# Optimization experiments

Measured on AMD Instinct MI355X. Metric: run time of the kernel, lower is better.

## Reference

```python
import jax, jax.numpy as jnp
import numpy as np

HEAD_SIZE = 64  # n_embds // n_heads = 1024 // 16

def setup_inputs() -> dict:
    key = jax.random.key(0)
    k0, k1, k2, k3 = jax.random.split(key, 4)
    B, S, D, H = 4, 4096, 1024, HEAD_SIZE
    scale = 1.0 / np.sqrt(D)
    return {
        "decoder_input": jax.random.normal(k0, (B, S, D), dtype=jnp.float32),
        "Wq": jax.random.normal(k1, (D, H), dtype=jnp.float32) * scale,
        "Wk": jax.random.normal(k2, (D, H), dtype=jnp.float32) * scale,
        "Wv": jax.random.normal(k3, (D, H), dtype=jnp.float32) * scale,
    }

def reference(decoder_input, Wq, Wk, Wv):
    # q,k,v: [B,S,H]; Linear(bias=False) == x @ W
    q = decoder_input @ Wq
    k = decoder_input @ Wk
    v = decoder_input @ Wv
    head_size = k.shape[2]
    # scores: [B,S,S] -- full materialization, as in the original
    scores = jnp.einsum('bqh,bkh->bqk', q, k) / jnp.sqrt(jnp.float32(head_size))
    S = scores.shape[1]
    causal = jnp.tril(jnp.ones((S, S), dtype=bool))  # lower-triangular mask
    masked = jnp.where(causal, scores, -jnp.inf)
    attn = jax.nn.softmax(masked, axis=2)
    # dropout_rate = 0.0 -> identity
    return jnp.einsum('bqk,bkh->bqh', attn, v)
```

## Files before the change

kernel.cpp:

```cpp
#include <hip/hip_runtime.h>
#include <hip/hip_bf16.h>
#include <math.h>

typedef __bf16 bf16_t;
typedef __bf16 bf16x8 __attribute__((ext_vector_type(8)));
typedef float f32x4 __attribute__((ext_vector_type(4)));

constexpr int SS = 4096;
constexpr int DD = 1024;
constexpr int HH = 64;

#if __has_builtin(__builtin_amdgcn_exp2f)
#define EXP2F __builtin_amdgcn_exp2f
#else
#define EXP2F exp2f
#endif

static __device__ __forceinline__ f32x4 mfma16(bf16x8 a, bf16x8 b, f32x4 c) {
  return __builtin_amdgcn_mfma_f32_16x16x32_bf16(a, b, c, 0, 0, 0);
}

__global__ __launch_bounds__(256) void prep_w(const float* __restrict__ wq,
                                              const float* __restrict__ wk,
                                              const float* __restrict__ wv,
                                              bf16_t* __restrict__ wt) {
  __shared__ float ls[64 * 68];
  int tid = threadIdx.x;
  int sel = blockIdx.x >> 4, kb = blockIdx.x & 15, k0 = kb * 64;
  const float* src = (sel == 0) ? wq : ((sel == 1) ? wk : wv);
  int bn = sel * 64;
#pragma unroll
  for (int i = 0; i < 4; ++i) {
    int e = tid + i * 256;
    int r = e >> 4, c4 = (e & 15) * 4;
    *(float4*)&ls[r * 68 + c4] = *(const float4*)(src + (size_t)(k0 + r) * 64 + c4);
  }
  __syncthreads();
#pragma unroll
  for (int j = 0; j < 2; ++j) {
    int e = tid + j * 256;
    int n = e >> 3, kg = e & 7;
    bf16x8 v;
#pragma unroll
    for (int t = 0; t < 8; ++t) v[t] = (bf16_t)ls[(kg * 8 + t) * 68 + n];
    *(bf16x8*)(wt + (size_t)(bn + n) * 1024 + k0 + kg * 8) = v;
  }
}

__global__ __launch_bounds__(256) void gemm_qkv(const float* __restrict__ x,
                                                const bf16_t* __restrict__ wt,
                                                bf16_t* __restrict__ qo,
                                                bf16_t* __restrict__ ko,
                                                bf16_t* __restrict__ vto) {
  __shared__ bf16_t xs[2][32 * 64];
  __shared__ bf16_t wsh[2][96 * 64];
  int tid = threadIdx.x;
  int wave = tid >> 6, lane = tid & 63, quad = lane >> 4, ml = lane & 15;
  int mh = wave >> 1, nh = wave & 1;
  int mblk = blockIdx.x >> 1, nhalf = blockIdx.x & 1;
  int m0 = mblk * 32;
  int nbase = nhalf * 96;

  f32x4 acc[3];
#pragma unroll
  for (int i = 0; i < 3; ++i) acc[i] = (f32x4){0.f, 0.f, 0.f, 0.f};

  int srow = tid >> 3, scc = tid & 7;
  float4 xr[2];
  bf16x8 wr[3];

  auto load_g = [&](int k0) {
    const float* p = x + (size_t)(m0 + srow) * DD + k0 + scc * 8;
    xr[0] = *(const float4*)p;
    xr[1] = *(const float4*)(p + 4);
#pragma unroll
    for (int i = 0; i < 3; ++i) {
      int c = tid + i * 256;
      int r = c >> 3, cc = c & 7;
      wr[i] = *(const bf16x8*)(wt + (size_t)(nbase + r) * DD + k0 + cc * 8);
    }
  };
  auto store_lds = [&](int bf) {
    bf16x8 v;
    v[0] = (bf16_t)xr[0].x; v[1] = (bf16_t)xr[0].y;
    v[2] = (bf16_t)xr[0].z; v[3] = (bf16_t)xr[0].w;
    v[4] = (bf16_t)xr[1].x; v[5] = (bf16_t)xr[1].y;
    v[6] = (bf16_t)xr[1].z; v[7] = (bf16_t)xr[1].w;
    *(bf16x8*)&xs[bf][srow * 64 + ((scc ^ (srow & 7)) * 8)] = v;
#pragma unroll
    for (int i = 0; i < 3; ++i) {
      int c = tid + i * 256;
      int r = c >> 3, cc = c & 7;
      *(bf16x8*)&wsh[bf][r * 64 + ((cc ^ (r & 7)) * 8)] = wr[i];
    }
  };

  load_g(0);
  store_lds(0);
  load_g(64);
  __syncthreads();
  for (int it = 0; it < 16; ++it) {
    int bf = it & 1;
#pragma unroll
    for (int s = 0; s < 2; ++s) {
      int rchunk = ((s * 4 + quad) ^ (ml & 7)) * 8;
      bf16x8 a = *(const bf16x8*)&xs[bf][(mh * 16 + ml) * 64 + rchunk];
#pragma unroll
      for (int i = 0; i < 3; ++i) {
        bf16x8 bfr = *(const bf16x8*)&wsh[bf][(nh * 48 + i * 16 + ml) * 64 + rchunk];
        acc[i] = mfma16(a, bfr, acc[i]);
      }
    }
    if (it < 15) {
      store_lds(1 - bf);
      if (it < 14) load_g((it + 2) * 64);
      __syncthreads();
    }
  }

  int b = m0 >> 12;
  int sr = m0 & 4095;
  const float QSCALE = 0.18033688011112042f;
  bf16_t* vls = (bf16_t*)xs;
  __syncthreads();
#pragma unroll
  for (int i = 0; i < 3; ++i) {
    int col = nbase + nh * 48 + i * 16 + ml;
#pragma unroll
    for (int r = 0; r < 4; ++r) {
      int lrow = mh * 16 + quad * 4 + r;
      size_t grow = (size_t)b * SS + sr + lrow;
      if (col < 64) qo[grow * HH + col] = (bf16_t)(acc[i][r] * QSCALE);
      else if (col < 128) ko[grow * HH + (col - 64)] = (bf16_t)(acc[i][r]);
      else vls[(col - 128) * 40 + lrow] = (bf16_t)(acc[i][r]);
    }
  }
  if (nhalf == 1) {
    __syncthreads();
    int h = tid >> 2, sg = tid & 3;
    *(bf16x8*)(vto + ((size_t)b * HH + h) * SS + sr + sg * 8) =
        *(const bf16x8*)&vls[h * 40 + sg * 8];
  }
}

__global__ __launch_bounds__(256) void attn_partial(const bf16_t* __restrict__ qg,
                                                    const bf16_t* __restrict__ kg,
                                                    const bf16_t* __restrict__ vg,
                                                    float* __restrict__ partO,
                                                    float* __restrict__ lb,
                                                    float* __restrict__ out) {
  __shared__ bf16_t Kl[64 * 64];
  __shared__ bf16_t Vl[64 * 64];
  __shared__ bf16_t Pl[4][16 * 64];
  int tid = threadIdx.x;
  int wave = tid >> 6, lane = tid & 63, quad = lane >> 4, ml = lane & 15;

  int bid = blockIdx.x;
  int b, jt, c0, len, slot = 0;
  bool direct;
  if (bid < 768) {
    jt = 63 - (bid >> 4);
    int rem = bid & 15;
    b = rem >> 2;
    int ch = rem & 3;
    int L = (jt + 4) >> 2;
    c0 = ch * L;
    int c1 = c0 + L; if (c1 > jt + 1) c1 = jt + 1;
    len = c1 - c0;
    slot = (b * 48 + (jt - 16)) * 4 + ch;
    direct = false;
  } else {
    int idx = bid - 768;
    jt = 15 - (idx >> 2);
    b = idx & 3;
    c0 = 0;
    len = jt + 1;
    direct = true;
  }
  int q0 = jt * 64;

  const bf16_t* qb = qg + (size_t)b * SS * HH;
  const bf16_t* kb = kg + (size_t)b * SS * HH;
  const bf16_t* vb = vg + (size_t)b * HH * SS;

  int qrow = q0 + wave * 16 + ml;
  bf16x8 aq0 = *(const bf16x8*)(qb + (size_t)qrow * HH + quad * 8);
  bf16x8 aq1 = *(const bf16x8*)(qb + (size_t)qrow * HH + 32 + quad * 8);

  bf16x8 kreg[2], vreg[2];
  int srl = tid >> 3, scc = tid & 7;
  auto load_kv = [&](int kt) {
#pragma unroll
    for (int i = 0; i < 2; ++i) {
      int r = srl + i * 32;
      kreg[i] = *(const bf16x8*)(kb + (size_t)(kt * 64 + r) * HH + scc * 8);
      vreg[i] = *(const bf16x8*)(vb + (size_t)r * SS + kt * 64 + scc * 8);
    }
  };
  auto store_kv = [&]() {
#pragma unroll
    for (int i = 0; i < 2; ++i) {
      int r = srl + i * 32;
      int off = r * 64 + ((scc ^ (r & 7)) * 8);
      *(bf16x8*)&Kl[off] = kreg[i];
      *(bf16x8*)&Vl[off] = vreg[i];
    }
  };

  f32x4 oa[4];
#pragma unroll
  for (int i = 0; i < 4; ++i) oa[i] = (f32x4){0.f, 0.f, 0.f, 0.f};
  float lr[4] = {0.f, 0.f, 0.f, 0.f};

  load_kv(c0);
  store_kv();

  for (int i = 0; i < len; ++i) {
    int kt = c0 + i;
    __syncthreads();
    if (i + 1 < len) load_kv(kt + 1);

    f32x4 sa[4];
#pragma unroll
    for (int nt = 0; nt < 4; ++nt) sa[nt] = (f32x4){0.f, 0.f, 0.f, 0.f};
#pragma unroll
    for (int s = 0; s < 2; ++s) {
      bf16x8 a = s ? aq1 : aq0;
      int rchunk = ((s * 4 + quad) ^ (ml & 7)) * 8;
#pragma unroll
      for (int nt = 0; nt < 4; ++nt) {
        bf16x8 bfr = *(const bf16x8*)&Kl[(nt * 16 + ml) * 64 + rchunk];
        sa[nt] = mfma16(a, bfr, sa[nt]);
      }
    }

    if (kt == jt) {
#pragma unroll
      for (int nt = 0; nt < 4; ++nt) {
        int key = kt * 64 + nt * 16 + ml;
#pragma unroll
        for (int r = 0; r < 4; ++r) {
          int qr = q0 + wave * 16 + quad * 4 + r;
          if (key > qr) sa[nt][r] = -3.38953139e38f;
        }
      }
    }

#pragma unroll
    for (int r = 0; r < 4; ++r) {
      float p0 = EXP2F(sa[0][r]);
      float p1 = EXP2F(sa[1][r]);
      float p2 = EXP2F(sa[2][r]);
      float p3 = EXP2F(sa[3][r]);
      sa[0][r] = p0; sa[1][r] = p1; sa[2][r] = p2; sa[3][r] = p3;
      lr[r] += (p0 + p1) + (p2 + p3);
    }

#pragma unroll
    for (int nt = 0; nt < 4; ++nt) {
#pragma unroll
      for (int r = 0; r < 4; ++r) {
        int row = quad * 4 + r;
        int cc = nt * 2 + (ml >> 3);
        Pl[wave][row * 64 + ((cc ^ (row & 7)) * 8) + (ml & 7)] = (bf16_t)sa[nt][r];
      }
    }
#pragma unroll
    for (int s = 0; s < 2; ++s) {
      int rchunk = ((s * 4 + quad) ^ (ml & 7)) * 8;
      bf16x8 pa = *(const bf16x8*)&Pl[wave][ml * 64 + rchunk];
#pragma unroll
      for (int ht = 0; ht < 4; ++ht) {
        bf16x8 bv = *(const bf16x8*)&Vl[(ht * 16 + ml) * 64 + rchunk];
        oa[ht] = mfma16(pa, bv, oa[ht]);
      }
    }

    __syncthreads();
    if (i + 1 < len) store_kv();
  }

#pragma unroll
  for (int r = 0; r < 4; ++r) {
    float t = lr[r];
    t += __shfl_xor(t, 1);
    t += __shfl_xor(t, 2);
    t += __shfl_xor(t, 4);
    t += __shfl_xor(t, 8);
    lr[r] = t;
  }

  if (direct) {
#pragma unroll
    for (int r = 0; r < 4; ++r) {
      float inv = 1.0f / lr[r];
      int row = q0 + wave * 16 + quad * 4 + r;
#pragma unroll
      for (int ht = 0; ht < 4; ++ht)
        out[((size_t)b * SS + row) * HH + ht * 16 + ml] = oa[ht][r] * inv;
    }
  } else {
    float* po = partO + (size_t)slot * 4096;
#pragma unroll
    for (int r = 0; r < 4; ++r) {
      int row = wave * 16 + quad * 4 + r;
#pragma unroll
      for (int ht = 0; ht < 4; ++ht)
        po[row * 64 + ht * 16 + ml] = oa[ht][r];
      if (ml == 0) lb[slot * 64 + row] = lr[r];
    }
  }
}

__global__ __launch_bounds__(256) void combine(const float* __restrict__ partO,
                                               const float* __restrict__ lb,
                                               float* __restrict__ out) {
  int bid = blockIdx.x;
  int b = bid / 96;
  int rest = bid - b * 96;
  int jt = 16 + (rest >> 1), half = rest & 1;
  int base = (b * 48 + (jt - 16)) * 4;
  int tid = threadIdx.x;
  int lr_ = tid >> 3, cb = tid & 7;
  int row = half * 32 + lr_;

  float l = 0.f;
  float4 o0 = {0.f, 0.f, 0.f, 0.f}, o1 = {0.f, 0.f, 0.f, 0.f};
#pragma unroll
  for (int c = 0; c < 4; ++c) {
    l += lb[(base + c) * 64 + row];
    const float* p = partO + (size_t)(base + c) * 4096 + row * 64 + cb * 8;
    float4 a = *(const float4*)p;
    float4 bq = *(const float4*)(p + 4);
    o0.x += a.x; o0.y += a.y; o0.z += a.z; o0.w += a.w;
    o1.x += bq.x; o1.y += bq.y; o1.z += bq.z; o1.w += bq.w;
  }
  float inv = 1.0f / l;
  float* op = out + (((size_t)b * SS) + jt * 64 + row) * HH + cb * 8;
  o0.x *= inv; o0.y *= inv; o0.z *= inv; o0.w *= inv;
  o1.x *= inv; o1.y *= inv; o1.z *= inv; o1.w *= inv;
  *(float4*)op = o0;
  *(float4*)(op + 4) = o1;
}

extern "C" void kernel_launch(void* const* d_in, const int* in_sizes, int n_in,
                              void* d_out, int out_size, void* d_ws, size_t ws_size,
                              hipStream_t stream) {
  const float* x  = (const float*)d_in[0];
  const float* wq = (const float*)d_in[1];
  const float* wk = (const float*)d_in[2];
  const float* wv = (const float*)d_in[3];
  float* out = (float*)d_out;

  char* wsb = (char*)d_ws;
  bf16_t* wt  = (bf16_t*)wsb;
  bf16_t* q   = (bf16_t*)(wsb + 524288);
  bf16_t* k   = (bf16_t*)(wsb + 2621440);
  bf16_t* vt  = (bf16_t*)(wsb + 4718592);
  float*  po  = (float*)(wsb + 6815744);
  float*  lb  = (float*)(wsb + 19398656);

  prep_w<<<48, 256, 0, stream>>>(wq, wk, wv, wt);
  gemm_qkv<<<1024, 256, 0, stream>>>(x, wt, q, k, vt);
  attn_partial<<<832, 256, 0, stream>>>(q, k, vt, po, lb, out);
  combine<<<384, 256, 0, stream>>>(po, lb, out);
}
```

Baseline: 155.8 us.

## Split attention KV into fixed 8-tile chunks with double-buffered LDS

```diff
diff --git a/kernel.cpp b/kernel.cpp
--- a/kernel.cpp
+++ b/kernel.cpp
@@ -149,34 +149,21 @@
                                                     float* __restrict__ partO,
                                                     float* __restrict__ lb,
                                                     float* __restrict__ out) {
-  __shared__ bf16_t Kl[64 * 64];
-  __shared__ bf16_t Vl[64 * 64];
+  __shared__ bf16_t Kl[2][64 * 64];
+  __shared__ bf16_t Vl[2][64 * 64];
   __shared__ bf16_t Pl[4][16 * 64];
   int tid = threadIdx.x;
   int wave = tid >> 6, lane = tid & 63, quad = lane >> 4, ml = lane & 15;
 
   int bid = blockIdx.x;
-  int b, jt, c0, len, slot = 0;
-  bool direct;
-  if (bid < 768) {
-    jt = 63 - (bid >> 4);
-    int rem = bid & 15;
-    b = rem >> 2;
-    int ch = rem & 3;
-    int L = (jt + 4) >> 2;
-    c0 = ch * L;
-    int c1 = c0 + L; if (c1 > jt + 1) c1 = jt + 1;
-    len = c1 - c0;
-    slot = (b * 48 + (jt - 16)) * 4 + ch;
-    direct = false;
-  } else {
-    int idx = bid - 768;
-    jt = 15 - (idx >> 2);
-    b = idx & 3;
-    c0 = 0;
-    len = jt + 1;
-    direct = true;
-  }
+  int jt = 63 - (bid >> 5);
+  int b = (bid >> 3) & 3;
+  int ch = bid & 7;
+  int nch = (jt >> 3) + 1;
+  if (ch >= nch) return;
+  int c0 = ch * 8;
+  int len = min(8, jt + 1 - c0);
+  bool direct = (nch == 1);
   int q0 = jt * 64;
 
   const bf16_t* qb = qg + (size_t)b * SS * HH;
@@ -197,13 +184,13 @@
       vreg[i] = *(const bf16x8*)(vb + (size_t)r * SS + kt * 64 + scc * 8);
     }
   };
-  auto store_kv = [&]() {
+  auto store_kv = [&](int bf) {
 #pragma unroll
     for (int i = 0; i < 2; ++i) {
       int r = srl + i * 32;
       int off = r * 64 + ((scc ^ (r & 7)) * 8);
-      *(bf16x8*)&Kl[off] = kreg[i];
-      *(bf16x8*)&Vl[off] = vreg[i];
+      *(bf16x8*)&Kl[bf][off] = kreg[i];
+      *(bf16x8*)&Vl[bf][off] = vreg[i];
     }
   };
 
@@ -213,10 +200,11 @@
   float lr[4] = {0.f, 0.f, 0.f, 0.f};
 
   load_kv(c0);
-  store_kv();
+  store_kv(0);
 
   for (int i = 0; i < len; ++i) {
     int kt = c0 + i;
+    int bf = i & 1;
     __syncthreads();
     if (i + 1 < len) load_kv(kt + 1);
 
@@ -229,7 +217,7 @@
       int rchunk = ((s * 4 + quad) ^ (ml & 7)) * 8;
 #pragma unroll
       for (int nt = 0; nt < 4; ++nt) {
-        bf16x8 bfr = *(const bf16x8*)&Kl[(nt * 16 + ml) * 64 + rchunk];
+        bf16x8 bfr = *(const bf16x8*)&Kl[bf][(nt * 16 + ml) * 64 + rchunk];
         sa[nt] = mfma16(a, bfr, sa[nt]);
       }
     }
@@ -271,13 +259,12 @@
       bf16x8 pa = *(const bf16x8*)&Pl[wave][ml * 64 + rchunk];
 #pragma unroll
       for (int ht = 0; ht < 4; ++ht) {
-        bf16x8 bv = *(const bf16x8*)&Vl[(ht * 16 + ml) * 64 + rchunk];
+        bf16x8 bv = *(const bf16x8*)&Vl[bf][(ht * 16 + ml) * 64 + rchunk];
         oa[ht] = mfma16(pa, bv, oa[ht]);
       }
     }
 
-    __syncthreads();
-    if (i + 1 < len) store_kv();
+    if (i + 1 < len) store_kv(1 - bf);
   }
 
 #pragma unroll
@@ -300,6 +287,7 @@
         out[((size_t)b * SS + row) * HH + ht * 16 + ml] = oa[ht][r] * inv;
     }
   } else {
+    int slot = (b << 9) + (jt << 3) + ch;
     float* po = partO + (size_t)slot * 4096;
 #pragma unroll
     for (int r = 0; r < 4; ++r) {
@@ -316,31 +304,27 @@
                                                const float* __restrict__ lb,
                                                float* __restrict__ out) {
   int bid = blockIdx.x;
-  int b = bid / 96;
-  int rest = bid - b * 96;
-  int jt = 16 + (rest >> 1), half = rest & 1;
-  int base = (b * 48 + (jt - 16)) * 4;
+  int b = bid / 56;
+  int jt = 8 + (bid - b * 56);
+  int nch = (jt >> 3) + 1;
+  int base = (b << 9) + (jt << 3);
   int tid = threadIdx.x;
-  int lr_ = tid >> 3, cb = tid & 7;
-  int row = half * 32 + lr_;
+  int row = tid >> 2, cb = tid & 3;
 
   float l = 0.f;
-  float4 o0 = {0.f, 0.f, 0.f, 0.f}, o1 = {0.f, 0.f, 0.f, 0.f};
-#pragma unroll
-  for (int c = 0; c < 4; ++c) {
+  f32x4 o[4];
+#pragma unroll
+  for (int j = 0; j < 4; ++j) o[j] = (f32x4){0.f, 0.f, 0.f, 0.f};
+  for (int c = 0; c < nch; ++c) {
     l += lb[(base + c) * 64 + row];
-    const float* p = partO + (size_t)(base + c) * 4096 + row * 64 + cb * 8;
-    float4 a = *(const float4*)p;
-    float4 bq = *(const float4*)(p + 4);
-    o0.x += a.x; o0.y += a.y; o0.z += a.z; o0.w += a.w;
-    o1.x += bq.x; o1.y += bq.y; o1.z += bq.z; o1.w += bq.w;
+    const f32x4* p = (const f32x4*)(partO + (size_t)(base + c) * 4096 + row * 64 + cb * 16);
+#pragma unroll
+    for (int j = 0; j < 4; ++j) o[j] += p[j];
   }
   float inv = 1.0f / l;
-  float* op = out + (((size_t)b * SS) + jt * 64 + row) * HH + cb * 8;
-  o0.x *= inv; o0.y *= inv; o0.z *= inv; o0.w *= inv;
-  o1.x *= inv; o1.y *= inv; o1.z *= inv; o1.w *= inv;
-  *(float4*)op = o0;
-  *(float4*)(op + 4) = o1;
+  f32x4* op = (f32x4*)(out + (((size_t)b * SS) + jt * 64 + row) * HH + cb * 16);
+#pragma unroll
+  for (int j = 0; j < 4; ++j) op[j] = o[j] * inv;
 }
 
 extern "C" void kernel_launch(void* const* d_in, const int* in_sizes, int n_in,
@@ -358,10 +342,10 @@
   bf16_t* k   = (bf16_t*)(wsb + 2621440);
   bf16_t* vt  = (bf16_t*)(wsb + 4718592);
   float*  po  = (float*)(wsb + 6815744);
-  float*  lb  = (float*)(wsb + 19398656);
+  float*  lb  = (float*)(wsb + 40370176);
 
   prep_w<<<48, 256, 0, stream>>>(wq, wk, wv, wt);
   gemm_qkv<<<1024, 256, 0, stream>>>(x, wt, q, k, vt);
-  attn_partial<<<832, 256, 0, stream>>>(q, k, vt, po, lb, out);
-  combine<<<384, 256, 0, stream>>>(po, lb, out);
-}
+  attn_partial<<<2048, 256, 0, stream>>>(q, k, vt, po, lb, out);
+  combine<<<224, 256, 0, stream>>>(po, lb, out);
+}
```

After: 160.7 us. 1.03x slower.

## Enlarge QKV GEMM M-tile to 64 rows and double-buffer K/V in attention

Applied to the files above, without the earlier changes.

```diff
diff --git a/kernel.cpp b/kernel.cpp
--- a/kernel.cpp
+++ b/kernel.cpp
@@ -52,27 +52,28 @@
                                                 bf16_t* __restrict__ qo,
                                                 bf16_t* __restrict__ ko,
                                                 bf16_t* __restrict__ vto) {
-  __shared__ bf16_t xs[2][32 * 64];
+  __shared__ bf16_t xs[2][64 * 64];
   __shared__ bf16_t wsh[2][96 * 64];
   int tid = threadIdx.x;
   int wave = tid >> 6, lane = tid & 63, quad = lane >> 4, ml = lane & 15;
-  int mh = wave >> 1, nh = wave & 1;
   int mblk = blockIdx.x >> 1, nhalf = blockIdx.x & 1;
-  int m0 = mblk * 32;
+  int m0 = mblk * 64;
   int nbase = nhalf * 96;
 
-  f32x4 acc[3];
-#pragma unroll
-  for (int i = 0; i < 3; ++i) acc[i] = (f32x4){0.f, 0.f, 0.f, 0.f};
-
-  int srow = tid >> 3, scc = tid & 7;
-  float4 xr[2];
+  f32x4 acc[6];
+#pragma unroll
+  for (int i = 0; i < 6; ++i) acc[i] = (f32x4){0.f, 0.f, 0.f, 0.f};
+
+  int xrow = tid >> 2, xseg = tid & 3;
+  float4 xr[4];
   bf16x8 wr[3];
 
   auto load_g = [&](int k0) {
-    const float* p = x + (size_t)(m0 + srow) * DD + k0 + scc * 8;
+    const float* p = x + (size_t)(m0 + xrow) * DD + k0 + xseg * 16;
     xr[0] = *(const float4*)p;
     xr[1] = *(const float4*)(p + 4);
+    xr[2] = *(const float4*)(p + 8);
+    xr[3] = *(const float4*)(p + 12);
 #pragma unroll
     for (int i = 0; i < 3; ++i) {
       int c = tid + i * 256;
@@ -81,12 +82,19 @@
     }
   };
   auto store_lds = [&](int bf) {
-    bf16x8 v;
-    v[0] = (bf16_t)xr[0].x; v[1] = (bf16_t)xr[0].y;
-    v[2] = (bf16_t)xr[0].z; v[3] = (bf16_t)xr[0].w;
-    v[4] = (bf16_t)xr[1].x; v[5] = (bf16_t)xr[1].y;
-    v[6] = (bf16_t)xr[1].z; v[7] = (bf16_t)xr[1].w;
-    *(bf16x8*)&xs[bf][srow * 64 + ((scc ^ (srow & 7)) * 8)] = v;
+    bf16x8 v0, v1;
+    v0[0] = (bf16_t)xr[0].x; v0[1] = (bf16_t)xr[0].y;
+    v0[2] = (bf16_t)xr[0].z; v0[3] = (bf16_t)xr[0].w;
+    v0[4] = (bf16_t)xr[1].x; v0[5] = (bf16_t)xr[1].y;
+    v0[6] = (bf16_t)xr[1].z; v0[7] = (bf16_t)xr[1].w;
+    v1[0] = (bf16_t)xr[2].x; v1[1] = (bf16_t)xr[2].y;
+    v1[2] = (bf16_t)xr[2].z; v1[3] = (bf16_t)xr[2].w;
+    v1[4] = (bf16_t)xr[3].x; v1[5] = (bf16_t)xr[3].y;
+    v1[6] = (bf16_t)xr[3].z; v1[7] = (bf16_t)xr[3].w;
+    int cc0 = (2 * xseg) ^ (xrow & 7);
+    int cc1 = (2 * xseg + 1) ^ (xrow & 7);
+    *(bf16x8*)&xs[bf][xrow * 64 + cc0 * 8] = v0;
+    *(bf16x8*)&xs[bf][xrow * 64 + cc1 * 8] = v1;
 #pragma unroll
     for (int i = 0; i < 3; ++i) {
       int c = tid + i * 256;
@@ -104,10 +112,10 @@
 #pragma unroll
     for (int s = 0; s < 2; ++s) {
       int rchunk = ((s * 4 + quad) ^ (ml & 7)) * 8;
-      bf16x8 a = *(const bf16x8*)&xs[bf][(mh * 16 + ml) * 64 + rchunk];
-#pragma unroll
-      for (int i = 0; i < 3; ++i) {
-        bf16x8 bfr = *(const bf16x8*)&wsh[bf][(nh * 48 + i * 16 + ml) * 64 + rchunk];
+      bf16x8 a = *(const bf16x8*)&xs[bf][(wave * 16 + ml) * 64 + rchunk];
+#pragma unroll
+      for (int i = 0; i < 6; ++i) {
+        bf16x8 bfr = *(const bf16x8*)&wsh[bf][(i * 16 + ml) * 64 + rchunk];
         acc[i] = mfma16(a, bfr, acc[i]);
       }
     }
@@ -121,25 +129,26 @@
   int b = m0 >> 12;
   int sr = m0 & 4095;
   const float QSCALE = 0.18033688011112042f;
-  bf16_t* vls = (bf16_t*)xs;
-  __syncthreads();
-#pragma unroll
-  for (int i = 0; i < 3; ++i) {
-    int col = nbase + nh * 48 + i * 16 + ml;
+  bf16_t* vls = (bf16_t*)wsh;
+#pragma unroll
+  for (int i = 0; i < 6; ++i) {
+    int col = nbase + i * 16 + ml;
 #pragma unroll
     for (int r = 0; r < 4; ++r) {
-      int lrow = mh * 16 + quad * 4 + r;
+      int lrow = wave * 16 + quad * 4 + r;
       size_t grow = (size_t)b * SS + sr + lrow;
       if (col < 64) qo[grow * HH + col] = (bf16_t)(acc[i][r] * QSCALE);
       else if (col < 128) ko[grow * HH + (col - 64)] = (bf16_t)(acc[i][r]);
-      else vls[(col - 128) * 40 + lrow] = (bf16_t)(acc[i][r]);
-    }
-  }
+      else vls[(col - 128) * 72 + lrow] = (bf16_t)(acc[i][r]);
+    }
+  }
+  __syncthreads();
   if (nhalf == 1) {
-    __syncthreads();
     int h = tid >> 2, sg = tid & 3;
-    *(bf16x8*)(vto + ((size_t)b * HH + h) * SS + sr + sg * 8) =
-        *(const bf16x8*)&vls[h * 40 + sg * 8];
+    *(bf16x8*)(vto + ((size_t)b * HH + h) * SS + sr + sg * 16) =
+        *(const bf16x8*)&vls[h * 72 + sg * 16];
+    *(bf16x8*)(vto + ((size_t)b * HH + h) * SS + sr + sg * 16 + 8) =
+        *(const bf16x8*)&vls[h * 72 + sg * 16 + 8];
   }
 }
 
@@ -149,8 +158,8 @@
                                                     float* __restrict__ partO,
                                                     float* __restrict__ lb,
                                                     float* __restrict__ out) {
-  __shared__ bf16_t Kl[64 * 64];
-  __shared__ bf16_t Vl[64 * 64];
+  __shared__ bf16_t Kl[2][64 * 64];
+  __shared__ bf16_t Vl[2][64 * 64];
   __shared__ bf16_t Pl[4][16 * 64];
   int tid = threadIdx.x;
   int wave = tid >> 6, lane = tid & 63, quad = lane >> 4, ml = lane & 15;
@@ -197,13 +206,13 @@
       vreg[i] = *(const bf16x8*)(vb + (size_t)r * SS + kt * 64 + scc * 8);
     }
   };
-  auto store_kv = [&]() {
+  auto store_kv = [&](int bf) {
 #pragma unroll
     for (int i = 0; i < 2; ++i) {
       int r = srl + i * 32;
       int off = r * 64 + ((scc ^ (r & 7)) * 8);
-      *(bf16x8*)&Kl[off] = kreg[i];
-      *(bf16x8*)&Vl[off] = vreg[i];
+      *(bf16x8*)&Kl[bf][off] = kreg[i];
+      *(bf16x8*)&Vl[bf][off] = vreg[i];
     }
   };
 
@@ -213,10 +222,11 @@
   float lr[4] = {0.f, 0.f, 0.f, 0.f};
 
   load_kv(c0);
-  store_kv();
+  store_kv(0);
 
   for (int i = 0; i < len; ++i) {
     int kt = c0 + i;
+    int bf = i & 1;
     __syncthreads();
     if (i + 1 < len) load_kv(kt + 1);
 
@@ -229,7 +239,7 @@
       int rchunk = ((s * 4 + quad) ^ (ml & 7)) * 8;
 #pragma unroll
       for (int nt = 0; nt < 4; ++nt) {
-        bf16x8 bfr = *(const bf16x8*)&Kl[(nt * 16 + ml) * 64 + rchunk];
+        bf16x8 bfr = *(const bf16x8*)&Kl[bf][(nt * 16 + ml) * 64 + rchunk];
         sa[nt] = mfma16(a, bfr, sa[nt]);
       }
     }
@@ -271,13 +281,12 @@
       bf16x8 pa = *(const bf16x8*)&Pl[wave][ml * 64 + rchunk];
 #pragma unroll
       for (int ht = 0; ht < 4; ++ht) {
-        bf16x8 bv = *(const bf16x8*)&Vl[(ht * 16 + ml) * 64 + rchunk];
+        bf16x8 bv = *(const bf16x8*)&Vl[bf][(ht * 16 + ml) * 64 + rchunk];
         oa[ht] = mfma16(pa, bv, oa[ht]);
       }
     }
 
-    __syncthreads();
-    if (i + 1 < len) store_kv();
+    if (i + 1 < len) store_kv(1 - bf);
   }
 
 #pragma unroll
@@ -361,7 +370,7 @@
   float*  lb  = (float*)(wsb + 19398656);
 
   prep_w<<<48, 256, 0, stream>>>(wq, wk, wv, wt);
-  gemm_qkv<<<1024, 256, 0, stream>>>(x, wt, q, k, vt);
+  gemm_qkv<<<512, 256, 0, stream>>>(x, wt, q, k, vt);
   attn_partial<<<832, 256, 0, stream>>>(q, k, vt, po, lb, out);
   combine<<<384, 256, 0, stream>>>(po, lb, out);
 }
```

New measurement: 151.4 us. 2.8% less time.

## Fuse all four stages into one cooperative persistent kernel with grid syncs

Applied to the files above, without the earlier changes.

```diff
diff --git a/kernel.cpp b/kernel.cpp
--- a/kernel.cpp
+++ b/kernel.cpp
@@ -1,6 +1,9 @@
 #include <hip/hip_runtime.h>
+#include <hip/hip_cooperative_groups.h>
 #include <hip/hip_bf16.h>
 #include <math.h>
+
+namespace cg = cooperative_groups;
 
 typedef __bf16 bf16_t;
 typedef __bf16 bf16x8 __attribute__((ext_vector_type(8)));
@@ -20,327 +23,341 @@
   return __builtin_amdgcn_mfma_f32_16x16x32_bf16(a, b, c, 0, 0, 0);
 }
 
-__global__ __launch_bounds__(256) void prep_w(const float* __restrict__ wq,
-                                              const float* __restrict__ wk,
-                                              const float* __restrict__ wv,
-                                              bf16_t* __restrict__ wt) {
-  __shared__ float ls[64 * 68];
-  int tid = threadIdx.x;
-  int sel = blockIdx.x >> 4, kb = blockIdx.x & 15, k0 = kb * 64;
-  const float* src = (sel == 0) ? wq : ((sel == 1) ? wk : wv);
-  int bn = sel * 64;
-#pragma unroll
-  for (int i = 0; i < 4; ++i) {
-    int e = tid + i * 256;
-    int r = e >> 4, c4 = (e & 15) * 4;
-    *(float4*)&ls[r * 68 + c4] = *(const float4*)(src + (size_t)(k0 + r) * 64 + c4);
-  }
-  __syncthreads();
-#pragma unroll
-  for (int j = 0; j < 2; ++j) {
-    int e = tid + j * 256;
-    int n = e >> 3, kg = e & 7;
-    bf16x8 v;
-#pragma unroll
-    for (int t = 0; t < 8; ++t) v[t] = (bf16_t)ls[(kg * 8 + t) * 68 + n];
-    *(bf16x8*)(wt + (size_t)(bn + n) * 1024 + k0 + kg * 8) = v;
-  }
-}
-
-__global__ __launch_bounds__(256) void gemm_qkv(const float* __restrict__ x,
-                                                const bf16_t* __restrict__ wt,
+__global__ __launch_bounds__(256, 4) void fused(const float* __restrict__ x,
+                                                const float* __restrict__ wq,
+                                                const float* __restrict__ wk,
+                                                const float* __restrict__ wv,
+                                                bf16_t* __restrict__ wt,
                                                 bf16_t* __restrict__ qo,
                                                 bf16_t* __restrict__ ko,
-                                                bf16_t* __restrict__ vto) {
-  __shared__ bf16_t xs[2][32 * 64];
-  __shared__ bf16_t wsh[2][96 * 64];
-  int tid = threadIdx.x;
-  int wave = tid >> 6, lane = tid & 63, quad = lane >> 4, ml = lane & 15;
-  int mh = wave >> 1, nh = wave & 1;
-  int mblk = blockIdx.x >> 1, nhalf = blockIdx.x & 1;
-  int m0 = mblk * 32;
-  int nbase = nhalf * 96;
-
-  f32x4 acc[3];
-#pragma unroll
-  for (int i = 0; i < 3; ++i) acc[i] = (f32x4){0.f, 0.f, 0.f, 0.f};
-
-  int srow = tid >> 3, scc = tid & 7;
-  float4 xr[2];
-  bf16x8 wr[3];
-
-  auto load_g = [&](int k0) {
-    const float* p = x + (size_t)(m0 + srow) * DD + k0 + scc * 8;
-    xr[0] = *(const float4*)p;
-    xr[1] = *(const float4*)(p + 4);
-#pragma unroll
-    for (int i = 0; i < 3; ++i) {
-      int c = tid + i * 256;
-      int r = c >> 3, cc = c & 7;
-      wr[i] = *(const bf16x8*)(wt + (size_t)(nbase + r) * DD + k0 + cc * 8);
-    }
-  };
-  auto store_lds = [&](int bf) {
-    bf16x8 v;
-    v[0] = (bf16_t)xr[0].x; v[1] = (bf16_t)xr[0].y;
-    v[2] = (bf16_t)xr[0].z; v[3] = (bf16_t)xr[0].w;
-    v[4] = (bf16_t)xr[1].x; v[5] = (bf16_t)xr[1].y;
-    v[6] = (bf16_t)xr[1].z; v[7] = (bf16_t)xr[1].w;
-    *(bf16x8*)&xs[bf][srow * 64 + ((scc ^ (srow & 7)) * 8)] = v;
-#pragma unroll
-    for (int i = 0; i < 3; ++i) {
-      int c = tid + i * 256;
-      int r = c >> 3, cc = c & 7;
-      *(bf16x8*)&wsh[bf][r * 64 + ((cc ^ (r & 7)) * 8)] = wr[i];
-    }
-  };
-
-  load_g(0);
-  store_lds(0);
-  load_g(64);
-  __syncthreads();
-  for (int it = 0; it < 16; ++it) {
-    int bf = it & 1;
-#pragma unroll
-    for (int s = 0; s < 2; ++s) {
-      int rchunk = ((s * 4 + quad) ^ (ml & 7)) * 8;
-      bf16x8 a = *(const bf16x8*)&xs[bf][(mh * 16 + ml) * 64 + rchunk];
-#pragma unroll
-      for (int i = 0; i < 3; ++i) {
-        bf16x8 bfr = *(const bf16x8*)&wsh[bf][(nh * 48 + i * 16 + ml) * 64 + rchunk];
-        acc[i] = mfma16(a, bfr, acc[i]);
-      }
-    }
-    if (it < 15) {
-      store_lds(1 - bf);
-      if (it < 14) load_g((it + 2) * 64);
+                                                bf16_t* __restrict__ vto,
+                                                float* __restrict__ partO,
+                                                float* __restrict__ lb,
+                                                float* __restrict__ out) {
+  __shared__ __align__(16) char smem[40960];
+  cg::grid_group grid = cg::this_grid();
+  const int nwg = gridDim.x;
+  const int wg = blockIdx.x;
+  const int tid = threadIdx.x;
+  const int wave = tid >> 6, lane = tid & 63, quad = lane >> 4, ml = lane & 15;
+
+  {
+    float* ls = (float*)smem;
+    for (int job = wg; job < 48; job += nwg) {
+      int sel = job >> 4, kb = job & 15, k0 = kb * 64;
+      const float* src = (sel == 0) ? wq : ((sel == 1) ? wk : wv);
+      int bn = sel * 64;
+#pragma unroll
+      for (int i = 0; i < 4; ++i) {
+        int e = tid + i * 256;
+        int r = e >> 4, c4 = (e & 15) * 4;
+        *(float4*)&ls[r * 68 + c4] = *(const float4*)(src + (size_t)(k0 + r) * 64 + c4);
+      }
+      __syncthreads();
+#pragma unroll
+      for (int j = 0; j < 2; ++j) {
+        int e = tid + j * 256;
+        int n = e >> 3, kg = e & 7;
+        bf16x8 v;
+#pragma unroll
+        for (int t = 0; t < 8; ++t) v[t] = (bf16_t)ls[(kg * 8 + t) * 68 + n];
+        *(bf16x8*)(wt + (size_t)(bn + n) * 1024 + k0 + kg * 8) = v;
+      }
       __syncthreads();
     }
   }
-
-  int b = m0 >> 12;
-  int sr = m0 & 4095;
-  const float QSCALE = 0.18033688011112042f;
-  bf16_t* vls = (bf16_t*)xs;
-  __syncthreads();
-#pragma unroll
-  for (int i = 0; i < 3; ++i) {
-    int col = nbase + nh * 48 + i * 16 + ml;
-#pragma unroll
-    for (int r = 0; r < 4; ++r) {
-      int lrow = mh * 16 + quad * 4 + r;
-      size_t grow = (size_t)b * SS + sr + lrow;
-      if (col < 64) qo[grow * HH + col] = (bf16_t)(acc[i][r] * QSCALE);
-      else if (col < 128) ko[grow * HH + (col - 64)] = (bf16_t)(acc[i][r]);
-      else vls[(col - 128) * 40 + lrow] = (bf16_t)(acc[i][r]);
+  grid.sync();
+
+  {
+    bf16_t* xs = (bf16_t*)smem;
+    bf16_t* wsh = (bf16_t*)(smem + 8192);
+    int mh = wave >> 1, nh = wave & 1;
+    int srow = tid >> 3, scc = tid & 7;
+
+    for (int job = wg; job < 1024; job += nwg) {
+      int mblk = job >> 1, nhalf = job & 1;
+      int m0 = mblk * 32;
+      int nbase = nhalf * 96;
+
+      f32x4 acc[3];
+#pragma unroll
+      for (int i = 0; i < 3; ++i) acc[i] = (f32x4){0.f, 0.f, 0.f, 0.f};
+
+      float4 xr[2];
+      bf16x8 wr[3];
+
+      auto load_g = [&](int k0) {
+        const float* p = x + (size_t)(m0 + srow) * DD + k0 + scc * 8;
+        xr[0] = *(const float4*)p;
+        xr[1] = *(const float4*)(p + 4);
+#pragma unroll
+        for (int i = 0; i < 3; ++i) {
+          int c = tid + i * 256;
+          int r = c >> 3, cc = c & 7;
+          wr[i] = *(const bf16x8*)(wt + (size_t)(nbase + r) * DD + k0 + cc * 8);
+        }
+      };
+      auto store_lds = [&](int bf) {
+        bf16x8 v;
+        v[0] = (bf16_t)xr[0].x; v[1] = (bf16_t)xr[0].y;
+        v[2] = (bf16_t)xr[0].z; v[3] = (bf16_t)xr[0].w;
+        v[4] = (bf16_t)xr[1].x; v[5] = (bf16_t)xr[1].y;
+        v[6] = (bf16_t)xr[1].z; v[7] = (bf16_t)xr[1].w;
+        *(bf16x8*)&xs[bf * 2048 + srow * 64 + ((scc ^ (srow & 7)) * 8)] = v;
+#pragma unroll
+        for (int i = 0; i < 3; ++i) {
+          int c = tid + i * 256;
+          int r = c >> 3, cc = c & 7;
+          *(bf16x8*)&wsh[bf * 6144 + r * 64 + ((cc ^ (r & 7)) * 8)] = wr[i];
+        }
+      };
+
+      load_g(0);
+      __syncthreads();
+      store_lds(0);
+      load_g(64);
+      __syncthreads();
+      for (int it = 0; it < 16; ++it) {
+        int bf = it & 1;
+#pragma unroll
+        for (int s = 0; s < 2; ++s) {
+          int rchunk = ((s * 4 + quad) ^ (ml & 7)) * 8;
+          bf16x8 a = *(const bf16x8*)&xs[bf * 2048 + (mh * 16 + ml) * 64 + rchunk];
+#pragma unroll
+          for (int i = 0; i < 3; ++i) {
+            bf16x8 bfr =
+                *(const bf16x8*)&wsh[bf * 6144 + (nh * 48 + i * 16 + ml) * 64 + rchunk];
+            acc[i] = mfma16(a, bfr, acc[i]);
+          }
+        }
+        if (it < 15) {
+          store_lds(1 - bf);
+          if (it < 14) load_g((it + 2) * 64);
+          __syncthreads();
+        }
+      }
+
+      int b = m0 >> 12;
+      int sr = m0 & 4095;
+      const float QSCALE = 0.18033688011112042f;
+      bf16_t* vls = xs;
+      __syncthreads();
+#pragma unroll
+      for (int i = 0; i < 3; ++i) {
+        int col = nbase + nh * 48 + i * 16 + ml;
+#pragma unroll
+        for (int r = 0; r < 4; ++r) {
+          int lrow = mh * 16 + quad * 4 + r;
+          size_t grow = (size_t)b * SS + sr + lrow;
+          if (col < 64) qo[grow * HH + col] = (bf16_t)(acc[i][r] * QSCALE);
+          else if (col < 128) ko[grow * HH + (col - 64)] = (bf16_t)(acc[i][r]);
+          else vls[(col - 128) * 40 + lrow] = (bf16_t)(acc[i][r]);
+        }
+      }
+      __syncthreads();
+      if (nhalf == 1) {
+        int h = tid >> 2, sg = tid & 3;
+        *(bf16x8*)(vto + ((size_t)b * HH + h) * SS + sr + sg * 8) =
+            *(const bf16x8*)&vls[h * 40 + sg * 8];
+      }
     }
   }
-  if (nhalf == 1) {
-    __syncthreads();
-    int h = tid >> 2, sg = tid & 3;
-    *(bf16x8*)(vto + ((size_t)b * HH + h) * SS + sr + sg * 8) =
-        *(const bf16x8*)&vls[h * 40 + sg * 8];
-  }
-}
-
-__global__ __launch_bounds__(256) void attn_partial(const bf16_t* __restrict__ qg,
-                                                    const bf16_t* __restrict__ kg,
-                                                    const bf16_t* __restrict__ vg,
-                                                    float* __restrict__ partO,
-                                                    float* __restrict__ lb,
-                                                    float* __restrict__ out) {
-  __shared__ bf16_t Kl[64 * 64];
-  __shared__ bf16_t Vl[64 * 64];
-  __shared__ bf16_t Pl[4][16 * 64];
-  int tid = threadIdx.x;
-  int wave = tid >> 6, lane = tid & 63, quad = lane >> 4, ml = lane & 15;
-
-  int bid = blockIdx.x;
-  int b, jt, c0, len, slot = 0;
-  bool direct;
-  if (bid < 768) {
-    jt = 63 - (bid >> 4);
-    int rem = bid & 15;
-    b = rem >> 2;
-    int ch = rem & 3;
-    int L = (jt + 4) >> 2;
-    c0 = ch * L;
-    int c1 = c0 + L; if (c1 > jt + 1) c1 = jt + 1;
-    len = c1 - c0;
-    slot = (b * 48 + (jt - 16)) * 4 + ch;
-    direct = false;
-  } else {
-    int idx = bid - 768;
-    jt = 15 - (idx >> 2);
-    b = idx & 3;
-    c0 = 0;
-    len = jt + 1;
-    direct = true;
-  }
-  int q0 = jt * 64;
-
-  const bf16_t* qb = qg + (size_t)b * SS * HH;
-  const bf16_t* kb = kg + (size_t)b * SS * HH;
-  const bf16_t* vb = vg + (size_t)b * HH * SS;
-
-  int qrow = q0 + wave * 16 + ml;
-  bf16x8 aq0 = *(const bf16x8*)(qb + (size_t)qrow * HH + quad * 8);
-  bf16x8 aq1 = *(const bf16x8*)(qb + (size_t)qrow * HH + 32 + quad * 8);
-
-  bf16x8 kreg[2], vreg[2];
-  int srl = tid >> 3, scc = tid & 7;
-  auto load_kv = [&](int kt) {
-#pragma unroll
-    for (int i = 0; i < 2; ++i) {
-      int r = srl + i * 32;
-      kreg[i] = *(const bf16x8*)(kb + (size_t)(kt * 64 + r) * HH + scc * 8);
-      vreg[i] = *(const bf16x8*)(vb + (size_t)r * SS + kt * 64 + scc * 8);
-    }
-  };
-  auto store_kv = [&]() {
-#pragma unroll
-    for (int i = 0; i < 2; ++i) {
-      int r = srl + i * 32;
-      int off = r * 64 + ((scc ^ (r & 7)) * 8);
-      *(bf16x8*)&Kl[off] = kreg[i];
-      *(bf16x8*)&Vl[off] = vreg[i];
-    }
-  };
-
-  f32x4 oa[4];
-#pragma unroll
-  for (int i = 0; i < 4; ++i) oa[i] = (f32x4){0.f, 0.f, 0.f, 0.f};
-  float lr[4] = {0.f, 0.f, 0.f, 0.f};
-
-  load_kv(c0);
-  store_kv();
-
-  for (int i = 0; i < len; ++i) {
-    int kt = c0 + i;
-    __syncthreads();
-    if (i + 1 < len) load_kv(kt + 1);
-
-    f32x4 sa[4];
-#pragma unroll
-    for (int nt = 0; nt < 4; ++nt) sa[nt] = (f32x4){0.f, 0.f, 0.f, 0.f};
-#pragma unroll
-    for (int s = 0; s < 2; ++s) {
-      bf16x8 a = s ? aq1 : aq0;
-      int rchunk = ((s * 4 + quad) ^ (ml & 7)) * 8;
-#pragma unroll
-      for (int nt = 0; nt < 4; ++nt) {
-        bf16x8 bfr = *(const bf16x8*)&Kl[(nt * 16 + ml) * 64 + rchunk];
-        sa[nt] = mfma16(a, bfr, sa[nt]);
-      }
-    }
-
-    if (kt == jt) {
-#pragma unroll
-      for (int nt = 0; nt < 4; ++nt) {
-        int key = kt * 64 + nt * 16 + ml;
+  grid.sync();
+
+  {
+    bf16_t* Kl = (bf16_t*)smem;
+    bf16_t* Vl = (bf16_t*)(smem + 16384);
+    bf16_t* Pl = (bf16_t*)(smem + 32768);
+    int srl = tid >> 3, scc = tid & 7;
+
+    for (int job = wg; job < 832; job += nwg) {
+      int b, jt, c0, len, slot = 0;
+      bool direct;
+      if (job < 768) {
+        jt = 63 - (job >> 4);
+        int rem = job & 15;
+        b = rem >> 2;
+        int ch = rem & 3;
+        int L = (jt + 4) >> 2;
+        c0 = ch * L;
+        int c1 = c0 + L; if (c1 > jt + 1) c1 = jt + 1;
+        len = c1 - c0;
+        slot = (b * 48 + (jt - 16)) * 4 + ch;
+        direct = false;
+      } else {
+        int idx = job - 768;
+        jt = 15 - (idx >> 2);
+        b = idx & 3;
+        c0 = 0;
+        len = jt + 1;
+        direct = true;
+      }
+      int q0 = jt * 64;
+
+      const bf16_t* qb = qo + (size_t)b * SS * HH;
+      const bf16_t* kb = ko + (size_t)b * SS * HH;
+      const bf16_t* vb = vto + (size_t)b * HH * SS;
+
+      int qrow = q0 + wave * 16 + ml;
+      bf16x8 aq0 = *(const bf16x8*)(qb + (size_t)qrow * HH + quad * 8);
+      bf16x8 aq1 = *(const bf16x8*)(qb + (size_t)qrow * HH + 32 + quad * 8);
+
+      bf16x8 kreg[2], vreg[2];
+      auto load_kv = [&](int kt) {
+#pragma unroll
+        for (int i = 0; i < 2; ++i) {
+          int r = srl + i * 32;
+          kreg[i] = *(const bf16x8*)(kb + (size_t)(kt * 64 + r) * HH + scc * 8);
+          vreg[i] = *(const bf16x8*)(vb + (size_t)r * SS + kt * 64 + scc * 8);
+        }
+      };
+      auto store_kv = [&](int bf) {
+#pragma unroll
+        for (int i = 0; i < 2; ++i) {
+          int r = srl + i * 32;
+          int off = r * 64 + ((scc ^ (r & 7)) * 8);
+          *(bf16x8*)&Kl[bf * 4096 + off] = kreg[i];
+          *(bf16x8*)&Vl[bf * 4096 + off] = vreg[i];
+        }
+      };
+
+      f32x4 oa[4];
+#pragma unroll
+      for (int i = 0; i < 4; ++i) oa[i] = (f32x4){0.f, 0.f, 0.f, 0.f};
+      float lr[4] = {0.f, 0.f, 0.f, 0.f};
+
+      load_kv(c0);
+      __syncthreads();
+      store_kv(0);
+
+      for (int i = 0; i < len; ++i) {
+        int kt = c0 + i;
+        int bf = i & 1;
+        __syncthreads();
+        if (i + 1 < len) load_kv(kt + 1);
+
+        f32x4 sa[4];
+#pragma unroll
+        for (int nt = 0; nt < 4; ++nt) sa[nt] = (f32x4){0.f, 0.f, 0.f, 0.f};
+#pragma unroll
+        for (int s = 0; s < 2; ++s) {
+          bf16x8 a = s ? aq1 : aq0;
+          int rchunk = ((s * 4 + quad) ^ (ml & 7)) * 8;
+#pragma unroll
+          for (int nt = 0; nt < 4; ++nt) {
+            bf16x8 bfr = *(const bf16x8*)&Kl[bf * 4096 + (nt * 16 + ml) * 64 + rchunk];
+            sa[nt] = mfma16(a, bfr, sa[nt]);
+          }
+        }
+
+        if (kt == jt) {
+#pragma unroll
+          for (int nt = 0; nt < 4; ++nt) {
+            int key = kt * 64 + nt * 16 + ml;
+#pragma unroll
+            for (int r = 0; r < 4; ++r) {
+              int qr = q0 + wave * 16 + quad * 4 + r;
+              if (key > qr) sa[nt][r] = -3.38953139e38f;
+            }
+          }
+        }
+
 #pragma unroll
         for (int r = 0; r < 4; ++r) {
-          int qr = q0 + wave * 16 + quad * 4 + r;
-          if (key > qr) sa[nt][r] = -3.38953139e38f;
-        }
-      }
-    }
-
-#pragma unroll
-    for (int r = 0; r < 4; ++r) {
-      float p0 = EXP2F(sa[0][r]);
-      float p1 = EXP2F(sa[1][r]);
-      float p2 = EXP2F(sa[2][r]);
-      float p3 = EXP2F(sa[3][r]);
-      sa[0][r] = p0; sa[1][r] = p1; sa[2][r] = p2; sa[3][r] = p3;
-      lr[r] += (p0 + p1) + (p2 + p3);
-    }
-
-#pragma unroll
-    for (int nt = 0; nt < 4; ++nt) {
+          float p0 = EXP2F(sa[0][r]);
+          float p1 = EXP2F(sa[1][r]);
+          float p2 = EXP2F(sa[2][r]);
+          float p3 = EXP2F(sa[3][r]);
+          sa[0][r] = p0; sa[1][r] = p1; sa[2][r] = p2; sa[3][r] = p3;
+          lr[r] += (p0 + p1) + (p2 + p3);
+        }
+
+#pragma unroll
+        for (int nt = 0; nt < 4; ++nt) {
+#pragma unroll
+          for (int r = 0; r < 4; ++r) {
+            int row = quad * 4 + r;
+            int cc = nt * 2 + (ml >> 3);
+            Pl[wave * 1024 + row * 64 + ((cc ^ (row & 7)) * 8) + (ml & 7)] =
+                (bf16_t)sa[nt][r];
+          }
+        }
+#pragma unroll
+        for (int s = 0; s < 2; ++s) {
+          int rchunk = ((s * 4 + quad) ^ (ml & 7)) * 8;
+          bf16x8 pa = *(const bf16x8*)&Pl[wave * 1024 + ml * 64 + rchunk];
+#pragma unroll
+          for (int ht = 0; ht < 4; ++ht) {
+            bf16x8 bv = *(const bf16x8*)&Vl[bf * 4096 + (ht * 16 + ml) * 64 + rchunk];
+            oa[ht] = mfma16(pa, bv, oa[ht]);
+          }
+        }
+
+        if (i + 1 < len) store_kv(1 - bf);
+      }
+
 #pragma unroll
       for (int r = 0; r < 4; ++r) {
-        int row = quad * 4 + r;
-        int cc = nt * 2 + (ml >> 3);
-        Pl[wave][row * 64 + ((cc ^ (row & 7)) * 8) + (ml & 7)] = (bf16_t)sa[nt][r];
-      }
-    }
-#pragma unroll
-    for (int s = 0; s < 2; ++s) {
-      int rchunk = ((s * 4 + quad) ^ (ml & 7)) * 8;
-      bf16x8 pa = *(const bf16x8*)&Pl[wave][ml * 64 + rchunk];
-#pragma unroll
-      for (int ht = 0; ht < 4; ++ht) {
-        bf16x8 bv = *(const bf16x8*)&Vl[(ht * 16 + ml) * 64 + rchunk];
-        oa[ht] = mfma16(pa, bv, oa[ht]);
-      }
-    }
-
-    __syncthreads();
-    if (i + 1 < len) store_kv();
-  }
-
-#pragma unroll
-  for (int r = 0; r < 4; ++r) {
-    float t = lr[r];
-    t += __shfl_xor(t, 1);
-    t += __shfl_xor(t, 2);
-    t += __shfl_xor(t, 4);
-    t += __shfl_xor(t, 8);
-    lr[r] = t;
-  }
-
-  if (direct) {
-#pragma unroll
-    for (int r = 0; r < 4; ++r) {
-      float inv = 1.0f / lr[r];
-      int row = q0 + wave * 16 + quad * 4 + r;
-#pragma unroll
-      for (int ht = 0; ht < 4; ++ht)
-        out[((size_t)b * SS + row) * HH + ht * 16 + ml] = oa[ht][r] * inv;
-    }
-  } else {
-    float* po = partO + (size_t)slot * 4096;
-#pragma unroll
-    for (int r = 0; r < 4; ++r) {
-      int row = wave * 16 + quad * 4 + r;
-#pragma unroll
-      for (int ht = 0; ht < 4; ++ht)
-        po[row * 64 + ht * 16 + ml] = oa[ht][r];
-      if (ml == 0) lb[slot * 64 + row] = lr[r];
+        float t = lr[r];
+        t += __shfl_xor(t, 1);
+        t += __shfl_xor(t, 2);
+        t += __shfl_xor(t, 4);
+        t += __shfl_xor(t, 8);
+        lr[r] = t;
+      }
+
+      if (direct) {
+#pragma unroll
+        for (int r = 0; r < 4; ++r) {
+          float inv = 1.0f / lr[r];
+          int row = q0 + wave * 16 + quad * 4 + r;
+#pragma unroll
+          for (int ht = 0; ht < 4; ++ht)
+            out[((size_t)b * SS + row) * HH + ht * 16 + ml] = oa[ht][r] * inv;
+        }
+      } else {
+        float* po = partO + (size_t)slot * 4096;
+#pragma unroll
+        for (int r = 0; r < 4; ++r) {
+          int row = wave * 16 + quad * 4 + r;
+#pragma unroll
+          for (int ht = 0; ht < 4; ++ht)
+            po[row * 64 + ht * 16 + ml] = oa[ht][r];
+          if (ml == 0) lb[slot * 64 + row] = lr[r];
+        }
+      }
     }
   }
-}
-
-__global__ __launch_bounds__(256) void combine(const float* __restrict__ partO,
-                                               const float* __restrict__ lb,
-                                               float* __restrict__ out) {
-  int bid = blockIdx.x;
-  int b = bid / 96;
-  int rest = bid - b * 96;
-  int jt = 16 + (rest >> 1), half = rest & 1;
-  int base = (b * 48 + (jt - 16)) * 4;
-  int tid = threadIdx.x;
-  int lr_ = tid >> 3, cb = tid & 7;
-  int row = half * 32 + lr_;
-
-  float l = 0.f;
-  float4 o0 = {0.f, 0.f, 0.f, 0.f}, o1 = {0.f, 0.f, 0.f, 0.f};
-#pragma unroll
-  for (int c = 0; c < 4; ++c) {
-    l += lb[(base + c) * 64 + row];
-    const float* p = partO + (size_t)(base + c) * 4096 + row * 64 + cb * 8;
-    float4 a = *(const float4*)p;
-    float4 bq = *(const float4*)(p + 4);
-    o0.x += a.x; o0.y += a.y; o0.z += a.z; o0.w += a.w;
-    o1.x += bq.x; o1.y += bq.y; o1.z += bq.z; o1.w += bq.w;
+  grid.sync();
+
+  {
+    for (int job = wg; job < 384; job += nwg) {
+      int b = job / 96;
+      int rest = job - b * 96;
+      int jt = 16 + (rest >> 1), half = rest & 1;
+      int base = (b * 48 + (jt - 16)) * 4;
+      int lr_ = tid >> 3, cb = tid & 7;
+      int row = half * 32 + lr_;
+
+      float l = 0.f;
+      float4 o0 = {0.f, 0.f, 0.f, 0.f}, o1 = {0.f, 0.f, 0.f, 0.f};
+#pragma unroll
+      for (int c = 0; c < 4; ++c) {
+        l += lb[(base + c) * 64 + row];
+        const float* p = partO + (size_t)(base + c) * 4096 + row * 64 + cb * 8;
+        float4 a = *(const float4*)p;
+        float4 bq = *(const float4*)(p + 4);
+        o0.x += a.x; o0.y += a.y; o0.z += a.z; o0.w += a.w;
+        o1.x += bq.x; o1.y += bq.y; o1.z += bq.z; o1.w += bq.w;
+      }
+      float inv = 1.0f / l;
+      float* op = out + (((size_t)b * SS) + jt * 64 + row) * HH + cb * 8;
+      o0.x *= inv; o0.y *= inv; o0.z *= inv; o0.w *= inv;
+      o1.x *= inv; o1.y *= inv; o1.z *= inv; o1.w *= inv;
+      *(float4*)op = o0;
+      *(float4*)(op + 4) = o1;
+    }
   }
-  float inv = 1.0f / l;
-  float* op = out + (((size_t)b * SS) + jt * 64 + row) * HH + cb * 8;
-  o0.x *= inv; o0.y *= inv; o0.z *= inv; o0.w *= inv;
-  o1.x *= inv; o1.y *= inv; o1.z *= inv; o1.w *= inv;
-  *(float4*)op = o0;
-  *(float4*)(op + 4) = o1;
 }
 
 extern "C" void kernel_launch(void* const* d_in, const int* in_sizes, int n_in,
@@ -360,8 +377,13 @@
   float*  po  = (float*)(wsb + 6815744);
   float*  lb  = (float*)(wsb + 19398656);
 
-  prep_w<<<48, 256, 0, stream>>>(wq, wk, wv, wt);
-  gemm_qkv<<<1024, 256, 0, stream>>>(x, wt, q, k, vt);
-  attn_partial<<<832, 256, 0, stream>>>(q, k, vt, po, lb, out);
-  combine<<<384, 256, 0, stream>>>(po, lb, out);
+  int occ = 0;
+  hipError_t e = hipOccupancyMaxActiveBlocksPerMultiprocessor(&occ, fused, 256, 0);
+  int nblk = (e == hipSuccess && occ > 0) ? occ * 256 : 512;
+  if (nblk > 1024) nblk = 1024;
+
+  void* args[] = {(void*)&x,  (void*)&wq, (void*)&wk, (void*)&wv, (void*)&wt,
+                  (void*)&q,  (void*)&k,  (void*)&vt, (void*)&po, (void*)&lb,
+                  (void*)&out};
+  hipLaunchCooperativeKernel(fused, dim3(nblk), dim3(256), args, 0, stream);
 }
```

New measurement: 344.8 us. 2.21x slower.
